# Kernel optimization log

Measured on AMD Instinct MI355X. Metric: run time of the kernel, lower is better.

The kernel has to match this reference:

```python
import jax, jax.numpy as jnp
import numpy as np

EPS = 1e-12


def pairwise_sqdist(x, y):
    # x: (B, N, 3), y: (B, M, 3) -> (B, N, M) squared euclidean distances
    xx = jnp.sum(x * x, axis=-1)              # (B, N)
    yy = jnp.sum(y * y, axis=-1)              # (B, M)
    xy = jnp.einsum('bnd,bmd->bnm', x, y)     # (B, N, M)
    d = xx[:, :, None] + yy[None_ if False else yy[:, None, :].shape and 0 or ...] if False else xx[:, :, None] + yy[:, None, :] - 2.0 * xy
    return jnp.maximum(d, 0.0)


def chamfer_l1(x, y):
    # pytorch3d/PoinTr-style ChamferDistanceL1:
    # mean over points of sqrt(min squared dist), averaged over both directions
    d = pairwise_sqdist(x, y)                 # (B, N, M)
    d1 = jnp.min(d, axis=2)                   # (B, N) x -> nearest y
    d2 = jnp.min(d, axis=1)                   # (B, M) y -> nearest x
    d1 = jnp.sqrt(jnp.maximum(d1, EPS))
    d2 = jnp.sqrt(jnp.maximum(d2, EPS))
    return 0.5 * (jnp.mean(d1) + jnp.mean(d2))


def knn1_gather(x, y):
    # For each point in x (B,N,3), find nearest neighbor in y (B,M,3) (K=1)
    # and gather it -> (B, N, 3). Matches knn_points + knn_gather + squeeze.
    d = pairwise_sqdist(x, y)                 # (B, N, M)
    idx = jnp.argmin(d, axis=2)               # (B, N) int
    return jnp.take_along_axis(y, idx[:, :, None], axis=1)  # (B, N, 3)


def volume_with_wedge(p):
    # wedge-product volume over consecutive point triples:
    # V = sum_i (p_i x p_{i+1}) . p_{i+2} / 6  -> (B,)
    c = jnp.cross(p[:, :-2, :], p[:, 1:-1, :])  # (B, N-2, 3)
    return jnp.sum(jnp.einsum('bnd,bnd->bn', c, p[:, 2:, :]), axis=-1) / 6.0


def setup_inputs() -> dict:
    key = jax.random.key(0)
    k1, k2, k3 = jax.random.split(key, 3)
    B, Nc, Nf, M = 2, 512, 8192, 8192
    return {
        'source_coarse': jax.random.normal(k1, (B, Nc, 3), dtype=jnp.float32),
        'source_fine': jax.random.normal(k2, (B, Nf, 3), dtype=jnp.float32),
        'target_points': jax.random.normal(k3, (B, M, 3), dtype=jnp.float32),
    }


def reference(source_coarse, source_fine, target_points):
    lambda_rot = lambda_ref = lambda_align = lambda_geo = 1.0
    B = source_fine.shape[0]
    axis = jnp.broadcast_to(jnp.array([0.0, 0.0, 1.0], dtype=source_fine.dtype), (B, 3))
    plane_normal = jnp.broadcast_to(jnp.array([0.0, 1.0, 0.0], dtype=source_fine.dtype), (B, 3))

    # KNN (K=1) gather of nearest target point for each fine source point
    new_target = knn1_gather(source_fine, target_points)  # (B, Nf, 3)

    # alignment (Chamfer L1) losses
    loss_align_coarse = chamfer_l1(source_coarse, target_points)
    loss_align_fine = chamfer_l1(source_fine, target_points)

    # rotational symmetry loss
    in_proj = jnp.einsum('bij,bj->bi', source_fine, axis)      # (B, Nf)
    re_proj = jnp.einsum('bij,bj->bi', new_target, axis)
    loss_rot = jnp.mean((jnp.linalg.norm(in_proj, axis=-1) - jnp.linalg.norm(re_proj, axis=-1)) ** 2)

    # reflectional symmetry loss
    pn = plane_normal / jnp.linalg.norm(plane_normal, axis=-1, keepdims=True)
    in_dist = jnp.einsum('bij,bj->bi', source_fine, pn)
    re_dist = jnp.einsum('bij,bj->bi', new_target, pn)
    loss_ref = jnp.mean((in_dist - re_dist) ** 2)

    # geometric consistency (wedge-product volume) loss
    loss_geo = jnp.mean((volume_with_wedge(source_fine) - volume_with_wedge(new_target)) ** 2)

    total = (lambda_rot * loss_rot + lambda_ref * loss_ref
             + lambda_align * loss_align_coarse + lambda_align * loss_align_fine
             + lambda_geo * loss_geo)
    return total
```

## Files before the change

kernel.cpp:

```cpp
#include <hip/hip_runtime.h>
#include <stdint.h>
#include <float.h>

using u64 = unsigned long long;
typedef float v2f __attribute__((ext_vector_type(2)));

constexpr int B_ = 2;
constexpr int NC = 512;
constexpr int NF = 8192;
constexpr int MT = 8192;

constexpr int TPB  = 256;
constexpr int RPB  = 512;
constexpr int TILE = 256;
constexpr int CF   = 16;
constexpr int TAIL_BLOCKS = 196;

#define DEVINL __device__ __forceinline__

template<bool ARGMIN>
DEVINL void pairmin_body(const float* __restrict__ P, const float* __restrict__ Q,
                         int nP, int nQ, int b, int row_base, int j0, int ntiles,
                         int chunk, int nRowsTot,
                         u64* __restrict__ outPack, unsigned* __restrict__ outVal,
                         float4* tile)
{
#pragma clang fp contract(off)
    const int tid  = threadIdx.x;
    const int row0 = row_base + tid;
    const int row1 = row_base + tid + TPB;
    const float* p0 = P + ((size_t)b * nP + row0) * 3;
    const float* p1 = P + ((size_t)b * nP + row1) * 3;
    float a0 = p0[0], a1 = p0[1], a2 = p0[2];
    float e0 = p1[0], e1 = p1[1], e2 = p1[2];
    v2f tx0 = {2.0f * a0, 2.0f * e0};
    v2f tx1 = {2.0f * a1, 2.0f * e1};
    v2f tx2 = {2.0f * a2, 2.0f * e2};
    v2f txx = {(a0*a0 + a1*a1) + a2*a2, (e0*e0 + e1*e1) + e2*e2};
    v2f dbest = {FLT_MAX, FLT_MAX};
    const v2f vzero = {0.0f, 0.0f};
    int jb0 = 0, jb1 = 0;

    for (int t = 0; t < ntiles; ++t) {
        __syncthreads();
        {
            const float* q = Q + ((size_t)b * nQ + j0 + t * TILE + tid) * 3;
            float q0 = q[0], q1 = q[1], q2 = q[2];
            tile[tid] = make_float4(q0, q1, q2, (q0*q0 + q1*q1) + q2*q2);
        }
        __syncthreads();
        const int jbase = j0 + t * TILE;
        for (int jj = 0; jj < TILE; jj += 4) {
            float4 qv[4];
            #pragma unroll
            for (int u = 0; u < 4; ++u) qv[u] = tile[jj + u];
            #pragma unroll
            for (int u = 0; u < 4; ++u) {
                v2f s  = (tx0 * qv[u].x + tx1 * qv[u].y) + tx2 * qv[u].z;
                v2f tt = txx + qv[u].w;
                v2f d  = tt - s;
                v2f dc = __builtin_elementwise_max(d, vzero);
                if (ARGMIN) {
                    int j = jbase + jj + u;
                    bool c0 = dc.x < dbest.x;
                    dbest.x = c0 ? dc.x : dbest.x;  jb0 = c0 ? j : jb0;
                    bool c1 = dc.y < dbest.y;
                    dbest.y = c1 ? dc.y : dbest.y;  jb1 = c1 ? j : jb1;
                } else {
                    dbest = __builtin_elementwise_min(dbest, dc);
                }
            }
        }
    }
    const size_t o0 = (size_t)chunk * nRowsTot + (size_t)b * nP;
    if (ARGMIN) {
        outPack[o0 + row0] = ((u64)__float_as_uint(dbest.x) << 32) | (unsigned)jb0;
        outPack[o0 + row1] = ((u64)__float_as_uint(dbest.y) << 32) | (unsigned)jb1;
    } else {
        outVal[o0 + row0] = __float_as_uint(dbest.x);
        outVal[o0 + row1] = __float_as_uint(dbest.y);
    }
}

__global__ __launch_bounds__(TPB, 8) void pairmin_all(
    const float* __restrict__ coarse, const float* __restrict__ fine,
    const float* __restrict__ tgt,
    u64* __restrict__ pfr, unsigned* __restrict__ pfc,
    unsigned* __restrict__ pcr, unsigned* __restrict__ pcc,
    unsigned* __restrict__ counter)
{
    __shared__ float4 tile[TILE];
    const int bx = blockIdx.x;
    if (bx == 0 && threadIdx.x == 0) *counter = 0;
    if (bx < 64) {
        int chunk = bx & 31, b = bx >> 5;
        pairmin_body<false>(coarse, tgt, NC, MT, b, 0, chunk * TILE, 1,
                            chunk, B_ * NC, nullptr, pcr, tile);
    } else if (bx < 128) {
        int i = bx - 64;
        int chunk = i & 1, yb = (i >> 1) & 15, b = i >> 5;
        pairmin_body<false>(tgt, coarse, MT, NC, b, yb * RPB, chunk * TILE, 1,
                            chunk, B_ * MT, nullptr, pcc, tile);
    } else if (bx < 640) {
        int i = bx - 128;
        int chunk = i & 15, yb = (i >> 4) & 15, b = i >> 8;
        pairmin_body<true>(fine, tgt, NF, MT, b, yb * RPB, chunk * (MT / CF), 2,
                           chunk, B_ * NF, pfr, nullptr, tile);
    } else {
        int i = bx - 640;
        int chunk = i & 15, yb = (i >> 4) & 15, b = i >> 8;
        pairmin_body<false>(tgt, fine, MT, NF, b, yb * RPB, chunk * (NF / CF), 2,
                            chunk, B_ * MT, nullptr, pfc, tile);
    }
}

__global__ __launch_bounds__(TPB) void tail_all(
    const float* __restrict__ fine, const float* __restrict__ tgt,
    const u64* __restrict__ pfr, const unsigned* __restrict__ pfc,
    const unsigned* __restrict__ pcr, const unsigned* __restrict__ pcc,
    double* __restrict__ bs, unsigned* __restrict__ counter,
    float* __restrict__ out)
{
    __shared__ float sp[TPB + 2][3], yp[TPB + 2][3];
    __shared__ double redw[4][9];
    __shared__ double lred[4][13];
    __shared__ int lastflag;
    const int bx = blockIdx.x, tid = threadIdx.x;
    const int wave = tid >> 6, lane = tid & 63;

    double v_s = 0, v_d2f = 0, v_d1c = 0, v_d2c = 0, v_yd2 = 0, v_zs = 0, v_zt = 0;
    double vs = 0, vt = 0;
    int role_b = 0;

    if (bx < 64) {
        const int base = bx * TPB;
        const int g = base + tid;
        const int b = base >> 13;  role_b = b;
        u64 best = pfr[g];
        #pragma unroll
        for (int c = 1; c < CF; ++c) {
            u64 p = pfr[(size_t)c * (B_ * NF) + g];
            best = p < best ? p : best;
        }
        float d1 = __uint_as_float((unsigned)(best >> 32));
        int idx  = (int)(best & 0xffffffffULL);
        float s = sqrtf(fmaxf(d1, 1e-12f));
        const float* y  = tgt  + ((size_t)b * MT + idx) * 3;
        const float* sr = fine + (size_t)g * 3;
        float y0 = y[0],  y1 = y[1],  y2 = y[2];
        float s0 = sr[0], s1 = sr[1], s2 = sr[2];
        yp[tid][0] = y0; yp[tid][1] = y1; yp[tid][2] = y2;
        sp[tid][0] = s0; sp[tid][1] = s1; sp[tid][2] = s2;
        const int base_b = base & (NF - 1);
        if (tid < 2 && base_b + TPB + tid < NF) {
            int g2 = base + TPB + tid;
            u64 b2 = pfr[g2];
            #pragma unroll
            for (int c = 1; c < CF; ++c) {
                u64 p = pfr[(size_t)c * (B_ * NF) + g2];
                b2 = p < b2 ? p : b2;
            }
            int i2 = (int)(b2 & 0xffffffffULL);
            const float* yh = tgt  + ((size_t)b * MT + i2) * 3;
            const float* sh = fine + (size_t)g2 * 3;
            #pragma unroll
            for (int k = 0; k < 3; ++k) { yp[TPB + tid][k] = yh[k]; sp[TPB + tid][k] = sh[k]; }
        }
        __syncthreads();
        v_s = s;
        float yd = s1 - y1;
        v_yd2 = (double)(yd * yd);
        v_zs  = (double)(s2 * s2);
        v_zt  = (double)(y2 * y2);
        int rb = base_b + tid;
        if (rb <= NF - 3) {
            {
                const float* a = sp[tid]; const float* c = sp[tid+1]; const float* e = sp[tid+2];
                float c0 = a[1]*c[2] - a[2]*c[1];
                float c1 = a[2]*c[0] - a[0]*c[2];
                float c2 = a[0]*c[1] - a[1]*c[0];
                vs = (double)(c0*e[0] + c1*e[1] + c2*e[2]);
            }
            {
                const float* a = yp[tid]; const float* c = yp[tid+1]; const float* e = yp[tid+2];
                float c0 = a[1]*c[2] - a[2]*c[1];
                float c1 = a[2]*c[0] - a[0]*c[2];
                float c2 = a[0]*c[1] - a[1]*c[0];
                vt = (double)(c0*e[0] + c1*e[1] + c2*e[2]);
            }
        }
    } else if (bx < 128) {
        const int g = (bx - 64) * TPB + tid;
        unsigned best = pfc[g];
        #pragma unroll
        for (int c = 1; c < CF; ++c) best = min(best, pfc[(size_t)c * (B_ * MT) + g]);
        v_d2f = (double)sqrtf(fmaxf(__uint_as_float(best), 1e-12f));
    } else if (bx < 132) {
        const int g = (bx - 128) * TPB + tid;
        unsigned best = pcr[g];
        #pragma unroll
        for (int c = 1; c < 32; ++c) best = min(best, pcr[(size_t)c * (B_ * NC) + g]);
        v_d1c = (double)sqrtf(fmaxf(__uint_as_float(best), 1e-12f));
    } else {
        const int g = (bx - 132) * TPB + tid;
        unsigned best = min(pcc[g], pcc[(size_t)(B_ * MT) + g]);
        v_d2c = (double)sqrtf(fmaxf(__uint_as_float(best), 1e-12f));
    }

    double r9[9] = {v_s, v_d2f, v_d1c, v_d2c, v_yd2, v_zs, v_zt, vs, vt};
    for (int o = 32; o; o >>= 1) {
        #pragma unroll
        for (int k = 0; k < 9; ++k) r9[k] += __shfl_down(r9[k], o);
    }
    if (lane == 0) {
        #pragma unroll
        for (int k = 0; k < 9; ++k) redw[wave][k] = r9[k];
    }
    __syncthreads();
    if (tid == 0) {
        double t9[9];
        #pragma unroll
        for (int k = 0; k < 9; ++k)
            t9[k] = redw[0][k] + redw[1][k] + redw[2][k] + redw[3][k];
        double* o = bs + (size_t)bx * 16;
        #pragma unroll
        for (int k = 0; k < 16; ++k) o[k] = 0.0;
        o[0] = t9[0]; o[1] = t9[1]; o[2] = t9[2]; o[3] = t9[3]; o[4] = t9[4];
        o[5 + role_b]  = t9[5];
        o[7 + role_b]  = t9[6];
        o[9 + role_b]  = t9[7];
        o[11 + role_b] = t9[8];
        __threadfence();
        unsigned old = atomicAdd(counter, 1u);
        lastflag = (old == TAIL_BLOCKS - 1);
    }
    __syncthreads();
    if (!lastflag) return;

    __threadfence();
    double c13[13];
    if (tid < TAIL_BLOCKS) {
        const double* p = bs + (size_t)tid * 16;
        #pragma unroll
        for (int k = 0; k < 13; ++k) c13[k] = p[k];
    } else {
        #pragma unroll
        for (int k = 0; k < 13; ++k) c13[k] = 0.0;
    }
    for (int o = 32; o; o >>= 1) {
        #pragma unroll
        for (int k = 0; k < 13; ++k) c13[k] += __shfl_down(c13[k], o);
    }
    if (lane == 0) {
        #pragma unroll
        for (int k = 0; k < 13; ++k) lred[wave][k] = c13[k];
    }
    __syncthreads();
    if (tid == 0) {
        double S[13];
        #pragma unroll
        for (int k = 0; k < 13; ++k)
            S[k] = lred[0][k] + lred[1][k] + lred[2][k] + lred[3][k];
        double m_d1f = S[0] / (double)(B_ * NF);
        double m_d2f = S[1] / (double)(B_ * MT);
        double m_d1c = S[2] / (double)(B_ * NC);
        double m_d2c = S[3] / (double)(B_ * MT);
        double loss_align_fine   = 0.5 * (m_d1f + m_d2f);
        double loss_align_coarse = 0.5 * (m_d1c + m_d2c);
        double loss_ref = S[4] / (double)(B_ * NF);
        double loss_rot = 0.0, loss_geo = 0.0;
        for (int b = 0; b < B_; ++b) {
            double dn = sqrt(S[5 + b]) - sqrt(S[7 + b]);
            loss_rot += dn * dn;
            double dv = (S[9 + b] - S[11 + b]) / 6.0;
            loss_geo += dv * dv;
        }
        loss_rot /= (double)B_;
        loss_geo /= (double)B_;
        out[0] = (float)(loss_rot + loss_ref + loss_align_coarse + loss_align_fine + loss_geo);
    }
}

extern "C" void kernel_launch(void* const* d_in, const int* in_sizes, int n_in,
                              void* d_out, int out_size, void* d_ws, size_t ws_size,
                              hipStream_t stream)
{
    const float* src_coarse = (const float*)d_in[0];
    const float* src_fine   = (const float*)d_in[1];
    const float* tgt        = (const float*)d_in[2];
    float* out = (float*)d_out;
    char*  ws  = (char*)d_ws;

    u64*      pfr     = (u64*)(ws);
    unsigned* pfc     = (unsigned*)(ws + 2097152);
    unsigned* pcr     = (unsigned*)(ws + 3145728);
    unsigned* pcc     = (unsigned*)(ws + 3276800);
    double*   bs      = (double*)(ws + 3407872);
    unsigned* counter = (unsigned*)(ws + 3432960);

    pairmin_all<<<dim3(1152), TPB, 0, stream>>>(
        src_coarse, src_fine, tgt, pfr, pfc, pcr, pcc, counter);
    tail_all<<<dim3(TAIL_BLOCKS), TPB, 0, stream>>>(
        src_fine, tgt, pfr, pfc, pcr, pcc, bs, counter, out);
}
```

Measured before the change: 130.3 us.

## Precompute padded point norms and stream block-uniform points from global memory instead of LDS

A new prep kernel packs fine, target and coarse points into float4 arrays with their squared norm, and also resets the counter. The pairwise-min loops then read these block-uniform points straight from global memory with a one-group register prefetch, dropping the shared-memory tiles and their barriers. The work split also changes: fine-column chunks go from 16 to 8, coarse rows use 16 chunks and coarse columns one, so there are 832 blocks and the tail reduction loops shrink to match. This adds one more kernel launch and relies on scalar or cached loads hiding global latency. The prefetch reads past the end of each chunk into the adjacent workspace, which is harmless but untidy.

```diff
diff --git a/kernel.cpp b/kernel.cpp
--- a/kernel.cpp
+++ b/kernel.cpp
@@ -10,20 +10,43 @@
 constexpr int NF = 8192;
 constexpr int MT = 8192;
 
-constexpr int TPB  = 256;
-constexpr int RPB  = 512;
-constexpr int TILE = 256;
-constexpr int CF   = 16;
+constexpr int TPB = 256;
+constexpr int RPB = 512;
+constexpr int CF  = 16;
+constexpr int CFC = 8;
 constexpr int TAIL_BLOCKS = 196;
 
 #define DEVINL __device__ __forceinline__
 
+__global__ __launch_bounds__(TPB) void prep(
+    const float* __restrict__ coarse, const float* __restrict__ fine,
+    const float* __restrict__ tgt,
+    float4* __restrict__ fine4, float4* __restrict__ tgt4,
+    float4* __restrict__ coarse4, unsigned* __restrict__ counter)
+{
+#pragma clang fp contract(off)
+    int g = blockIdx.x * TPB + threadIdx.x;
+    if (g == 0) *counter = 0;
+    if (g < B_ * NF) {
+        const float* p = fine + (size_t)g * 3;
+        float x = p[0], y = p[1], z = p[2];
+        fine4[g] = make_float4(x, y, z, (x*x + y*y) + z*z);
+        p = tgt + (size_t)g * 3;
+        x = p[0]; y = p[1]; z = p[2];
+        tgt4[g] = make_float4(x, y, z, (x*x + y*y) + z*z);
+        if (g < B_ * NC) {
+            p = coarse + (size_t)g * 3;
+            x = p[0]; y = p[1]; z = p[2];
+            coarse4[g] = make_float4(x, y, z, (x*x + y*y) + z*z);
+        }
+    }
+}
+
 template<bool ARGMIN>
-DEVINL void pairmin_body(const float* __restrict__ P, const float* __restrict__ Q,
-                         int nP, int nQ, int b, int row_base, int j0, int ntiles,
+DEVINL void pairmin_body(const float* __restrict__ P, const float4* __restrict__ Qf,
+                         int nP, int nQb, int b, int row_base, int j0, int jlen,
                          int chunk, int nRowsTot,
-                         u64* __restrict__ outPack, unsigned* __restrict__ outVal,
-                         float4* tile)
+                         u64* __restrict__ outPack, unsigned* __restrict__ outVal)
 {
 #pragma clang fp contract(off)
     const int tid  = threadIdx.x;
@@ -41,37 +64,32 @@
     const v2f vzero = {0.0f, 0.0f};
     int jb0 = 0, jb1 = 0;
 
-    for (int t = 0; t < ntiles; ++t) {
-        __syncthreads();
-        {
-            const float* q = Q + ((size_t)b * nQ + j0 + t * TILE + tid) * 3;
-            float q0 = q[0], q1 = q[1], q2 = q[2];
-            tile[tid] = make_float4(q0, q1, q2, (q0*q0 + q1*q1) + q2*q2);
-        }
-        __syncthreads();
-        const int jbase = j0 + t * TILE;
-        for (int jj = 0; jj < TILE; jj += 4) {
-            float4 qv[4];
-            #pragma unroll
-            for (int u = 0; u < 4; ++u) qv[u] = tile[jj + u];
-            #pragma unroll
-            for (int u = 0; u < 4; ++u) {
-                v2f s  = (tx0 * qv[u].x + tx1 * qv[u].y) + tx2 * qv[u].z;
-                v2f tt = txx + qv[u].w;
-                v2f d  = tt - s;
-                v2f dc = __builtin_elementwise_max(d, vzero);
-                if (ARGMIN) {
-                    int j = jbase + jj + u;
-                    bool c0 = dc.x < dbest.x;
-                    dbest.x = c0 ? dc.x : dbest.x;  jb0 = c0 ? j : jb0;
-                    bool c1 = dc.y < dbest.y;
-                    dbest.y = c1 ? dc.y : dbest.y;  jb1 = c1 ? j : jb1;
-                } else {
-                    dbest = __builtin_elementwise_min(dbest, dc);
-                }
+    const float4* Q = Qf + (size_t)b * nQb;
+    float4 c0 = Q[j0], c1 = Q[j0+1], c2 = Q[j0+2], c3 = Q[j0+3];
+
+    for (int j = j0; j < j0 + jlen; j += 4) {
+        float4 n0 = Q[j+4], n1 = Q[j+5], n2 = Q[j+6], n3 = Q[j+7];
+        float4 qg[4] = {c0, c1, c2, c3};
+        #pragma unroll
+        for (int u = 0; u < 4; ++u) {
+            float4 q = qg[u];
+            v2f s  = (tx0 * q.x + tx1 * q.y) + tx2 * q.z;
+            v2f tt = txx + q.w;
+            v2f d  = tt - s;
+            v2f dc = __builtin_elementwise_max(d, vzero);
+            if (ARGMIN) {
+                int jj = j + u;
+                bool g0 = dc.x < dbest.x;
+                dbest.x = g0 ? dc.x : dbest.x;  jb0 = g0 ? jj : jb0;
+                bool g1 = dc.y < dbest.y;
+                dbest.y = g1 ? dc.y : dbest.y;  jb1 = g1 ? jj : jb1;
+            } else {
+                dbest = __builtin_elementwise_min(dbest, dc);
             }
         }
-    }
+        c0 = n0; c1 = n1; c2 = n2; c3 = n3;
+    }
+
     const size_t o0 = (size_t)chunk * nRowsTot + (size_t)b * nP;
     if (ARGMIN) {
         outPack[o0 + row0] = ((u64)__float_as_uint(dbest.x) << 32) | (unsigned)jb0;
@@ -85,32 +103,31 @@
 __global__ __launch_bounds__(TPB, 8) void pairmin_all(
     const float* __restrict__ coarse, const float* __restrict__ fine,
     const float* __restrict__ tgt,
+    const float4* __restrict__ fine4, const float4* __restrict__ tgt4,
+    const float4* __restrict__ coarse4,
     u64* __restrict__ pfr, unsigned* __restrict__ pfc,
-    unsigned* __restrict__ pcr, unsigned* __restrict__ pcc,
-    unsigned* __restrict__ counter)
-{
-    __shared__ float4 tile[TILE];
+    unsigned* __restrict__ pcr, unsigned* __restrict__ pcc)
+{
     const int bx = blockIdx.x;
-    if (bx == 0 && threadIdx.x == 0) *counter = 0;
-    if (bx < 64) {
-        int chunk = bx & 31, b = bx >> 5;
-        pairmin_body<false>(coarse, tgt, NC, MT, b, 0, chunk * TILE, 1,
-                            chunk, B_ * NC, nullptr, pcr, tile);
-    } else if (bx < 128) {
-        int i = bx - 64;
-        int chunk = i & 1, yb = (i >> 1) & 15, b = i >> 5;
-        pairmin_body<false>(tgt, coarse, MT, NC, b, yb * RPB, chunk * TILE, 1,
-                            chunk, B_ * MT, nullptr, pcc, tile);
-    } else if (bx < 640) {
-        int i = bx - 128;
+    if (bx < 256) {
+        int chunk = bx & 7, yb = (bx >> 3) & 15, b = bx >> 7;
+        pairmin_body<false>(tgt, fine4, MT, NF, b, yb * RPB, chunk * 1024, 1024,
+                            chunk, B_ * MT, nullptr, pfc);
+    } else if (bx < 768) {
+        int i = bx - 256;
         int chunk = i & 15, yb = (i >> 4) & 15, b = i >> 8;
-        pairmin_body<true>(fine, tgt, NF, MT, b, yb * RPB, chunk * (MT / CF), 2,
-                           chunk, B_ * NF, pfr, nullptr, tile);
+        pairmin_body<true>(fine, tgt4, NF, MT, b, yb * RPB, chunk * 512, 512,
+                           chunk, B_ * NF, pfr, nullptr);
+    } else if (bx < 800) {
+        int i = bx - 768;
+        int chunk = i & 15, b = i >> 4;
+        pairmin_body<false>(coarse, tgt4, NC, MT, b, 0, chunk * 512, 512,
+                            chunk, B_ * NC, nullptr, pcr);
     } else {
-        int i = bx - 640;
-        int chunk = i & 15, yb = (i >> 4) & 15, b = i >> 8;
-        pairmin_body<false>(tgt, fine, MT, NF, b, yb * RPB, chunk * (NF / CF), 2,
-                            chunk, B_ * MT, nullptr, pfc, tile);
+        int i = bx - 800;
+        int yb = i & 15, b = i >> 4;
+        pairmin_body<false>(tgt, coarse4, MT, NC, b, yb * RPB, 0, 512,
+                            0, B_ * MT, nullptr, pcc);
     }
 }
 
@@ -193,18 +210,17 @@
         const int g = (bx - 64) * TPB + tid;
         unsigned best = pfc[g];
         #pragma unroll
-        for (int c = 1; c < CF; ++c) best = min(best, pfc[(size_t)c * (B_ * MT) + g]);
+        for (int c = 1; c < CFC; ++c) best = min(best, pfc[(size_t)c * (B_ * MT) + g]);
         v_d2f = (double)sqrtf(fmaxf(__uint_as_float(best), 1e-12f));
     } else if (bx < 132) {
         const int g = (bx - 128) * TPB + tid;
         unsigned best = pcr[g];
         #pragma unroll
-        for (int c = 1; c < 32; ++c) best = min(best, pcr[(size_t)c * (B_ * NC) + g]);
+        for (int c = 1; c < 16; ++c) best = min(best, pcr[(size_t)c * (B_ * NC) + g]);
         v_d1c = (double)sqrtf(fmaxf(__uint_as_float(best), 1e-12f));
     } else {
         const int g = (bx - 132) * TPB + tid;
-        unsigned best = min(pcc[g], pcc[(size_t)(B_ * MT) + g]);
-        v_d2c = (double)sqrtf(fmaxf(__uint_as_float(best), 1e-12f));
+        v_d2c = (double)sqrtf(fmaxf(__uint_as_float(pcc[g]), 1e-12f));
     }
 
     double r9[9] = {v_s, v_d2f, v_d1c, v_d2c, v_yd2, v_zs, v_zt, vs, vt};
@@ -293,13 +309,18 @@
 
     u64*      pfr     = (u64*)(ws);
     unsigned* pfc     = (unsigned*)(ws + 2097152);
-    unsigned* pcr     = (unsigned*)(ws + 3145728);
-    unsigned* pcc     = (unsigned*)(ws + 3276800);
-    double*   bs      = (double*)(ws + 3407872);
-    unsigned* counter = (unsigned*)(ws + 3432960);
-
-    pairmin_all<<<dim3(1152), TPB, 0, stream>>>(
-        src_coarse, src_fine, tgt, pfr, pfc, pcr, pcc, counter);
+    unsigned* pcr     = (unsigned*)(ws + 2621440);
+    unsigned* pcc     = (unsigned*)(ws + 2686976);
+    float4*   fine4   = (float4*)(ws + 2752512);
+    float4*   tgt4    = (float4*)(ws + 3014656);
+    float4*   coarse4 = (float4*)(ws + 3276800);
+    double*   bs      = (double*)(ws + 3293184);
+    unsigned* counter = (unsigned*)(ws + 3318272);
+
+    prep<<<dim3(64), TPB, 0, stream>>>(src_coarse, src_fine, tgt,
+                                       fine4, tgt4, coarse4, counter);
+    pairmin_all<<<dim3(832), TPB, 0, stream>>>(
+        src_coarse, src_fine, tgt, fine4, tgt4, coarse4, pfr, pfc, pcr, pcc);
     tail_all<<<dim3(TAIL_BLOCKS), TPB, 0, stream>>>(
         src_fine, tgt, pfr, pfc, pcr, pcc, bs, counter, out);
 }
```

Result: slower. 135.0 us (+3.6%).
